# Performance work log

Measured on AMD Instinct MI355X. Metric: run time of the kernel, lower is better.

The kernel has to match this reference:

```python
import jax, jax.numpy as jnp
import numpy as np

EPS = 1e-8


def setup_inputs() -> dict:
    key = jax.random.key(0)
    ks = jax.random.split(key, 3)
    B, d_in, d_sae = 2048, 2048, 16384
    x = jax.random.normal(ks[0], (B, 2, d_in), dtype=jnp.float32)
    W_enc = jax.random.normal(ks[1], (d_in, d_sae), dtype=jnp.float32) / (d_in ** 0.5)
    W_dec = jax.random.normal(ks[2], (d_sae, d_in), dtype=jnp.float32) / (d_sae ** 0.5)
    b_enc = jnp.zeros((d_sae,), dtype=jnp.float32)
    b_dec = jnp.zeros((d_in,), dtype=jnp.float32)
    return {"x": x, "W_enc": W_enc, "W_dec": W_dec, "b_enc": b_enc,
            "b_dec": b_dec, "k": 64, "h": 8192}


def _encode(x, W_enc, b_enc, k):
    # x: (N, d_in) -> z: (N, d_sae), top-k sparsified with relu on kept values
    pre = x @ W_enc + b_enc
    v, i = jax.lax.top_k(pre, k)                       # (N, k)
    rows = jnp.arange(pre.shape[0])[:, None]
    return jnp.zeros_like(pre).at[rows, i].set(jax.nn.relu(v))


def _info_nce(z_a, z_b):
    z_a = z_a / jnp.maximum(jnp.linalg.norm(z_a, axis=-1, keepdims=True), EPS)
    z_b = z_b / jnp.maximum(jnp.linalg.norm(z_b, axis=-1, keepdims=True), EPS)
    sim = z_a @ z_b.T                                  # (B, B)
    diag = jnp.diagonal(sim)
    ce_row = jnp.mean(jax.nn.logsumexp(sim, axis=1) - diag)
    ce_col = jnp.mean(jax.nn.logsumexp(sim, axis=0) - diag)
    return 0.5 * (ce_row + ce_col)


def reference(x, W_enc, W_dec, b_enc, b_dec, k, h):
    alpha = 1.0
    B, _, d_in = x.shape
    # encode both tokens in one GEMM: (2B, d_in)
    x_flat = x.reshape(B * 2, d_in)
    z = _encode(x_flat, W_enc, b_enc, k)               # (2B, d_sae)
    x_hat_full = z @ W_dec + b_dec                     # (2B, d_in)
    x_hat_high = z[:, :h] @ W_dec[:h, :] + b_dec       # (2B, d_in)
    per_tok = d_in
    # mean over batch per token, summed over prev+cur (matches 4 separate means)
    se_full = jnp.sum((x_hat_full - x_flat) ** 2, axis=-1).reshape(B, 2)
    se_high = jnp.sum((x_hat_high - x_flat) ** 2, axis=-1).reshape(B, 2)
    l_matr = (jnp.mean(se_full, axis=0).sum() + jnp.mean(se_high, axis=0).sum()) / per_tok
    z2 = z.reshape(B, 2, -1)
    z_h_prev = z2[:, 0, :h]
    z_h_cur = z2[:, 1, :h]
    l_contr = _info_nce(z_h_cur, z_h_prev)
    total = l_matr + alpha * l_contr
    x_hat_cur = x_hat_full.reshape(B, 2, d_in)[:, 1]
    z_cur = z2[:, 1]
    return (total, x_hat_cur, z_cur)
```

## Files before the change

### kernel.cpp

```cpp
#include <hip/hip_runtime.h>
#include <hip/hip_bf16.h>
#include <math.h>

#define D_IN   2048
#define D_SAE  16384
#define NROWS  4096
#define KTOP   64
#define HDIM   8192
#define CHUNK  1024
#define EPSN   1e-8f
#define BANDW_F16 4e-3f
#define BANDW_F32 4e-4f
#define BANDCAP 512
#define NTILE   128
#define SEG     16
#define CAPT    (NTILE*SEG)
#define TH_CAND 2.0f

typedef unsigned short u16;
typedef unsigned char u8;
typedef _Float16 f16;
typedef __attribute__((ext_vector_type(8))) _Float16 f16x8;
typedef __attribute__((ext_vector_type(4))) _Float16 f16x4;
typedef __attribute__((ext_vector_type(8))) unsigned short u16x8;
typedef __attribute__((ext_vector_type(4))) float float4v;
typedef __attribute__((ext_vector_type(2))) float f32x2;

__device__ __forceinline__ unsigned f2u(float f) {
  unsigned b = __float_as_uint(f);
  return (b & 0x80000000u) ? ~b : (b | 0x80000000u);
}
__device__ __forceinline__ float u2f(unsigned u) {
  unsigned b = (u & 0x80000000u) ? (u & 0x7fffffffu) : ~u;
  return __uint_as_float(b);
}
__device__ __forceinline__ u16 f2bf_rne(float f) {
  unsigned b = __float_as_uint(f);
  unsigned r = (b + 0x7fffu + ((b >> 16) & 1u)) >> 16;
  return (u16)r;
}
__device__ __forceinline__ float bf2f(u16 u) {
  return __uint_as_float(((unsigned)u) << 16);
}
__device__ __forceinline__ void async_copy16(void* lds, const void* g) {
  __builtin_amdgcn_global_load_lds(
      (const __attribute__((address_space(1))) unsigned*)(g),
      (__attribute__((address_space(3))) unsigned*)(lds), 16, 0, 0);
}

__global__ __launch_bounds__(256)
void pre_kernel(const float* __restrict__ x, const float* __restrict__ W,
                f16* __restrict__ Axh, f16* __restrict__ Th,
                float* __restrict__ WT)
{
  __shared__ float S[64][65];
  const int bid = blockIdx.x;
  if (bid < 8192) {
    const int tx = threadIdx.x & 63, ty = threadIdx.x >> 6;
    const int n0 = (bid & 255) * 64, k0 = (bid >> 8) * 64;
#pragma unroll
    for (int i = 0; i < 16; ++i) {
      int kl = ty + i * 4;
      S[kl][tx] = W[(size_t)(k0 + kl) * D_SAE + n0 + tx];
    }
    __syncthreads();
#pragma unroll
    for (int i = 0; i < 16; ++i) {
      int nl = ty + i * 4;
      float v = S[tx][nl];
      Th[(size_t)(n0 + nl) * D_IN + k0 + tx] = (f16)v;
      WT[(size_t)(n0 + nl) * D_IN + k0 + tx] = v;
    }
  } else {
    int t = (bid - 8192) * 256 + threadIdx.x;
    const int n4 = (NROWS * D_IN) / 4;
    if (t < n4) {
      float4 v = ((const float4*)x)[t];
      f16x4 h;
      h.x = (f16)v.x; h.y = (f16)v.y; h.z = (f16)v.z; h.w = (f16)v.w;
      ((f16x4*)Axh)[t] = h;
    }
  }
}

__global__ __launch_bounds__(256)
void wdec_to_fp8_kernel(const float* __restrict__ W,
                        u8* __restrict__ W8, float* __restrict__ scl)
{
  __shared__ float red[256];
  const int c = blockIdx.x;
  const int tid = threadIdx.x;
  const int e0 = tid * 8;
  const float* wr = W + (size_t)c * 2048;
  float4 a = *(const float4*)(wr + e0);
  float4 b = *(const float4*)(wr + e0 + 4);
  float w[8] = {a.x,a.y,a.z,a.w,b.x,b.y,b.z,b.w};
  float mx = 0.f;
#pragma unroll
  for (int i = 0; i < 8; ++i) mx = fmaxf(mx, fabsf(w[i]));
  red[tid] = mx; __syncthreads();
  for (int s = 128; s > 0; s >>= 1) { if (tid < s) red[tid] = fmaxf(red[tid], red[tid+s]); __syncthreads(); }
  const float mxa = red[0];
  const float senc = mxa > 0.f ? 448.f / mxa : 0.f;
  float q[8];
#pragma unroll
  for (int i = 0; i < 8; ++i) q[i] = fminf(fmaxf(w[i] * senc, -448.f), 448.f);
  int p0 = __builtin_amdgcn_cvt_pk_fp8_f32(q[0], q[1], 0, false);
  p0 = __builtin_amdgcn_cvt_pk_fp8_f32(q[2], q[3], p0, true);
  int p1 = __builtin_amdgcn_cvt_pk_fp8_f32(q[4], q[5], 0, false);
  p1 = __builtin_amdgcn_cvt_pk_fp8_f32(q[6], q[7], p1, true);
  uint2 o; o.x = (unsigned)p0; o.y = (unsigned)p1;
  *(uint2*)(W8 + (size_t)c * 2048 + e0) = o;
  if (tid == 0) scl[c] = mxa > 0.f ? mxa / 448.f : 0.f;
}

__global__ __launch_bounds__(256, 4)
void gemm_f16_kernel(const f16* __restrict__ Axh,
                     const f16* __restrict__ BT,
                     const float* __restrict__ bias,
                     unsigned* __restrict__ ckey_g,
                     u16* __restrict__ cidx_g,
                     unsigned* __restrict__ ccnt)
{
  __shared__ u16 sA[2][128 * 32];
  __shared__ u16 sB[2][128 * 32];
  const int tid = threadIdx.x;
  const int wave = tid >> 6, lane = tid & 63;
  const int bid = blockIdx.x;
  const int chunk = bid >> 10;
  const int b10 = bid & 1023;
  const int xcd = b10 & 7, loc = b10 >> 3;
  const int n0 = (xcd * 16 + (loc >> 3)) * 128;
  const int m0 = (loc & 7) * 128;
  const int row_base = chunk * CHUNK;
  const f16* A = Axh + (size_t)chunk * CHUNK * D_IN;
  const int wm = (wave >> 1) * 64, wn = (wave & 1) * 64;
  const int fr = lane & 15, fkg = lane >> 4;

  float4v acc[4][4];
#pragma unroll
  for (int i = 0; i < 4; ++i)
#pragma unroll
    for (int j = 0; j < 4; ++j) acc[i][j] = (float4v){0.f, 0.f, 0.f, 0.f};

  int aoff[4], boff[4];
#pragma unroll
  for (int mi = 0; mi < 4; ++mi) {
    int r = wm + mi * 16 + fr;
    aoff[mi] = r * 32 + ((fkg ^ ((r >> 1) & 3)) * 8);
    int c = wn + mi * 16 + fr;
    boff[mi] = c * 32 + ((fkg ^ ((c >> 1) & 3)) * 8);
  }

  auto stage = [&](int b, int k0) {
#pragma unroll
    for (int i = 0; i < 4; ++i) {
      int n = (i * 4 + wave) * 64 + lane;
      if (n < 512) {
        int row = n >> 2, s = n & 3;
        int fg = s ^ ((row >> 1) & 3);
        async_copy16((char*)&sA[b][0] + (size_t)n * 16,
                     A + (size_t)(m0 + row) * D_IN + k0 + fg * 8);
      } else {
        int n2 = n - 512;
        int row = n2 >> 2, s = n2 & 3;
        int fg = s ^ ((row >> 1) & 3);
        async_copy16((char*)&sB[b][0] + (size_t)n2 * 16,
                     BT + (size_t)(n0 + row) * D_IN + k0 + fg * 8);
      }
    }
  };

  stage(0, 0);
  __syncthreads();
  for (int t = 0; t < 64; ++t) {
    const int cur = t & 1;
    if (t < 63) stage(cur ^ 1, (t + 1) * 32);
    f16x8 a[4], b[4];
#pragma unroll
    for (int mi = 0; mi < 4; ++mi)
      a[mi] = *(const f16x8*)&sA[cur][aoff[mi]];
#pragma unroll
    for (int ni = 0; ni < 4; ++ni)
      b[ni] = *(const f16x8*)&sB[cur][boff[ni]];
#pragma unroll
    for (int mi = 0; mi < 4; ++mi)
#pragma unroll
      for (int ni = 0; ni < 4; ++ni)
        acc[mi][ni] = __builtin_amdgcn_mfma_f32_16x16x32_f16(a[mi], b[ni], acc[mi][ni], 0, 0, 0);
    __syncthreads();
  }

  unsigned* lcnt = (unsigned*)&sA[0][0];
  if (tid < 128) lcnt[tid] = 0u;
  __syncthreads();
  const int tileIdx = n0 >> 7;
  const int orow = (lane >> 4) * 4;
#pragma unroll
  for (int mi = 0; mi < 4; ++mi) {
#pragma unroll
    for (int ni = 0; ni < 4; ++ni) {
      int col = n0 + wn + ni * 16 + fr;
      float bv = bias[col];
#pragma unroll
      for (int rr = 0; rr < 4; ++rr) {
        float val = acc[mi][ni][rr] + bv;
        if (val >= TH_CAND) {
          int lrow = wm + mi * 16 + orow + rr;
          unsigned j = atomicAdd(&lcnt[lrow], 1u);
          if (j < SEG) {
            size_t sb = ((size_t)(row_base + m0 + lrow) * NTILE + tileIdx) * SEG;
            ckey_g[sb + j] = f2u(val);
            cidx_g[sb + j] = (u16)col;
          }
        }
      }
    }
  }
  __syncthreads();
  if (tid < 128)
    ccnt[(size_t)(row_base + m0 + tid) * NTILE + tileIdx] = lcnt[tid];
}

__global__ __launch_bounds__(256)
void select_compact_kernel(const unsigned* __restrict__ ckey_g,
                           const u16* __restrict__ cidx_g,
                           const unsigned* __restrict__ ccnt,
                           const float* __restrict__ x,
                           const float* __restrict__ WT,
                           const float* __restrict__ benc,
                           float bandw,
                           int*   __restrict__ topk_idx,
                           float* __restrict__ topk_val,
                           float* __restrict__ nh_norm,
                           unsigned* __restrict__ flags)
{
  __shared__ unsigned ckey[CAPT];
  __shared__ u16      cidx[CAPT];
  __shared__ unsigned tof[128];
  __shared__ unsigned tc[128];
  __shared__ unsigned hist[256];
  __shared__ unsigned sscan[257];
  __shared__ unsigned wsum[4];
  __shared__ float    bv_l[64];
  __shared__ int      band_idx[BANDCAP];
  __shared__ float    band_val[BANDCAP];
  __shared__ double   band_ex[BANDCAP];
  __shared__ unsigned char picked[BANDCAP];
  __shared__ int      out_idx[64];
  __shared__ float    out_val[64];
  __shared__ float    sh_v64;
  __shared__ unsigned sh_mcnt, sh_bstar, sh_kth, sh_ocnt, sh_bcnt, sh_bad;

  const int tid = threadIdx.x;
  const int wv = tid >> 6, ln = tid & 63;
  const int r = blockIdx.x;

  if (tid == 0) { sh_ocnt = 0u; sh_bcnt = 0u; sh_bad = 0u; sh_mcnt = 0u; sh_bstar = 0xffffffffu; }
  hist[tid] = 0u;
  if (tid < 128) {
    unsigned c = ccnt[(size_t)r * NTILE + tid];
    tc[tid] = c;
    if (c > SEG) sh_bad = 1u;
  }
  __syncthreads();
  if (tid < 128) {
    unsigned v = tc[tid];
#pragma unroll
    for (int d = 1; d < 64; d <<= 1) {
      unsigned t = __shfl_up(v, d);
      if (ln >= d) v += t;
    }
    tof[tid] = v;
  }
  __syncthreads();
  if (tid >= 64 && tid < 128) tof[tid] += tof[63];
  __syncthreads();
  const unsigned cc_u = tof[127];
  const int cc = (int)(cc_u < CAPT ? cc_u : CAPT);

  {
    unsigned ck[8]; u16 ci[8]; unsigned pv[8];
#pragma unroll
    for (int b = 0; b < 8; ++b) {
      int idx = tid + 256 * b;
      int tile = idx >> 4, slot = idx & 15;
      unsigned c = tc[tile]; if (c > SEG) c = SEG;
      bool valid = (unsigned)slot < c;
      pv[b] = valid ? (tof[tile] - tc[tile] + slot) : 0xffffffffu;
      ck[b] = valid ? ckey_g[(size_t)r * CAPT + idx] : 0u;
      ci[b] = valid ? cidx_g[(size_t)r * CAPT + idx] : (u16)0;
    }
#pragma unroll
    for (int b = 0; b < 8; ++b) {
      if (pv[b] < (unsigned)CAPT) { ckey[pv[b]] = ck[b]; cidx[pv[b]] = ci[b]; }
    }
  }
  __syncthreads();

  bool bad = (sh_bad != 0u) || (cc_u < 64u) || (cc_u > (unsigned)CAPT);

  if (!bad) {
    for (int s = tid; s < cc; s += 256) {
      float v = u2f(ckey[s]);
      int b = (int)((v - TH_CAND) * 100.0f);
      b = b < 0 ? 0 : (b > 255 ? 255 : b);
      atomicAdd(&hist[b], 1u);
    }
  }
  __syncthreads();
  {
    int rt = 255 - tid;
    unsigned v = hist[rt];
#pragma unroll
    for (int d = 1; d < 64; d <<= 1) {
      unsigned t = __shfl_up(v, d);
      if (ln >= d) v += t;
    }
    if (ln == 63) wsum[wv] = v;
    __syncthreads();
    unsigned add = 0;
    for (int w = 0; w < wv; ++w) add += wsum[w];
    sscan[rt] = v + add;
    if (tid == 0) sscan[256] = 0u;
    __syncthreads();
    if (sscan[tid] >= 64u && sscan[tid + 1] < 64u) {
      sh_bstar = (unsigned)tid;
      sh_kth = 64u - sscan[tid + 1];
    }
  }
  __syncthreads();

  if (bad || sh_bstar == 0xffffffffu) { if (tid == 0) flags[r] = 1u; return; }
  const int bstar = (int)sh_bstar;
  const unsigned kth = sh_kth;

  for (int s = tid; s < cc; s += 256) {
    float v = u2f(ckey[s]);
    int b = (int)((v - TH_CAND) * 100.0f);
    b = b < 0 ? 0 : (b > 255 ? 255 : b);
    if (b == bstar) {
      unsigned p = atomicAdd(&sh_mcnt, 1u);
      if (p < 64u) bv_l[p] = v;
    }
  }
  __syncthreads();
  if (sh_mcnt > 64u) { if (tid == 0) flags[r] = 1u; return; }
  const int m = (int)sh_mcnt;
  if (wv == 0 && ln < m) {
    float mine = bv_l[ln];
    int rank = 0;
    for (int j = 0; j < m; ++j) {
      float o = bv_l[j];
      if (o > mine || (o == mine && j < ln)) ++rank;
    }
    if (rank == (int)kth - 1) sh_v64 = mine;
  }
  __syncthreads();
  const float v64 = sh_v64;

  const float hi = v64 + 2.f * bandw, lo = v64 - 2.f * bandw;
  for (int s = tid; s < cc; s += 256) {
    float v = u2f(ckey[s]);
    int i = (int)cidx[s];
    if (v > hi) {
      unsigned p = atomicAdd(&sh_ocnt, 1u);
      out_idx[p] = i; out_val[p] = v;
    } else if (v >= lo) {
      unsigned p = atomicAdd(&sh_bcnt, 1u);
      if (p < BANDCAP) { band_idx[p] = i; band_val[p] = v; }
    }
  }
  __syncthreads();
  if (sh_bcnt > BANDCAP) { if (tid == 0) flags[r] = 1u; return; }
  const unsigned nci = sh_ocnt;
  const unsigned bcnt = sh_bcnt;
  const unsigned remaining = 64u - nci;

  if (bcnt == remaining) {
    for (unsigned s = tid; s < bcnt; s += 256) {
      out_idx[nci + s] = band_idx[s];
      out_val[nci + s] = band_val[s];
    }
    __syncthreads();
  } else {
    const float* xr = x + (size_t)r * 2048;
    for (unsigned bi = wv; bi < bcnt; bi += 4) {
      int c = band_idx[bi];
      const float* wr = WT + (size_t)c * 2048;
      double s = 0.0;
      for (int j0 = 0; j0 < 2048; j0 += 512) {
        float xa[8], wa[8];
#pragma unroll
        for (int u = 0; u < 8; ++u) {
          int j = j0 + ln + 64 * u;
          xa[u] = xr[j];
          wa[u] = wr[j];
        }
#pragma unroll
        for (int u = 0; u < 8; ++u)
          s += (double)xa[u] * (double)wa[u];
      }
#pragma unroll
      for (int off2 = 32; off2 > 0; off2 >>= 1)
        s += __shfl_down(s, off2);
      if (ln == 0) band_ex[bi] = s + (double)benc[c];
    }
    __syncthreads();
    if (tid == 0) {
      for (unsigned i2 = 0; i2 < bcnt; ++i2) picked[i2] = 0;
      for (unsigned s = 0; s < remaining; ++s) {
        int best = -1;
        for (unsigned b2 = 0; b2 < bcnt; ++b2) {
          if (picked[b2]) continue;
          if (best < 0 || band_ex[b2] > band_ex[best] ||
              (band_ex[b2] == band_ex[best] && band_idx[b2] < band_idx[best]))
            best = (int)b2;
        }
        picked[best] = 1;
        out_idx[nci + s] = band_idx[best];
        out_val[nci + s] = (float)band_ex[best];
      }
    }
    __syncthreads();
  }

  if (tid < 64) {
    float v = out_val[tid];
    v = v > 0.f ? v : 0.f;
    out_val[tid] = v;
    topk_idx[(size_t)r * 64 + tid] = out_idx[tid];
    topk_val[(size_t)r * 64 + tid] = v;
  }
  __syncthreads();
  if (tid == 0) {
    float n2 = 0.f;
    for (int s = 0; s < 64; ++s)
      if (out_idx[s] < HDIM) n2 += out_val[s] * out_val[s];
    nh_norm[r] = sqrtf(n2);
    flags[r] = 0u;
  }
}

__global__ __launch_bounds__(256)
void repair_kernel(const unsigned* __restrict__ flags,
                   const float* __restrict__ x,
                   const float* __restrict__ WT,
                   const float* __restrict__ benc,
                   int* __restrict__ topk_idx,
                   float* __restrict__ topk_val,
                   float* __restrict__ nh_norm)
{
  const int r = blockIdx.x;
  if (flags[r] == 0u) return;
  __shared__ float prerow[16384];
  __shared__ float xs[2048];
  __shared__ float rv[256];
  __shared__ int   ri[256];
  __shared__ int   oi[64];
  __shared__ float ov[64];
  const int tid = threadIdx.x;
  for (int i = tid; i < 2048; i += 256) xs[i] = x[(size_t)r * 2048 + i];
  __syncthreads();
  for (int c = tid; c < 16384; c += 256) {
    const float* wr = WT + (size_t)c * 2048;
    float s = 0.f;
    for (int j = 0; j < 2048; ++j) s = fmaf(xs[j], wr[j], s);
    prerow[c] = s + benc[c];
  }
  __syncthreads();
  for (int k2 = 0; k2 < 64; ++k2) {
    float bv = -INFINITY; int bi = 16384;
    for (int c = tid; c < 16384; c += 256) {
      float v = prerow[c];
      if (v > bv || (v == bv && c < bi)) { bv = v; bi = c; }
    }
    rv[tid] = bv; ri[tid] = bi;
    __syncthreads();
    for (int s2 = 128; s2 > 0; s2 >>= 1) {
      if (tid < s2) {
        if (rv[tid+s2] > rv[tid] || (rv[tid+s2] == rv[tid] && ri[tid+s2] < ri[tid])) {
          rv[tid] = rv[tid+s2]; ri[tid] = ri[tid+s2];
        }
      }
      __syncthreads();
    }
    if (tid == 0) { oi[k2] = ri[0]; ov[k2] = rv[0]; prerow[ri[0]] = -INFINITY; }
    __syncthreads();
  }
  if (tid < 64) {
    float v = ov[tid]; v = v > 0.f ? v : 0.f;
    topk_idx[(size_t)r * 64 + tid] = oi[tid];
    topk_val[(size_t)r * 64 + tid] = v;
  }
  __syncthreads();
  if (tid == 0) {
    float n2 = 0.f;
    for (int s = 0; s < 64; ++s)
      if (oi[s] < HDIM) { float v = ov[s] > 0.f ? ov[s] : 0.f; n2 += v * v; }
    nh_norm[r] = sqrtf(n2);
  }
}

__global__ __launch_bounds__(256)
void scatter_kernel(const int* __restrict__ topk_idx,
                    const float* __restrict__ topk_val,
                    const float* __restrict__ nh_norm,
                    float* __restrict__ zcur_out,
                    u16* __restrict__ ZpTb)
{
  int t = blockIdx.x * blockDim.x + threadIdx.x;
  if (t >= NROWS * 64) return;
  int r = t >> 6;
  int c = topk_idx[t];
  float v = topk_val[t];
  int b = r >> 1;
  if (r & 1) {
    zcur_out[(size_t)b * 16384 + c] = v;
  } else if (c < HDIM) {
    float nrm = nh_norm[r]; nrm = nrm > EPSN ? nrm : EPSN;
    ZpTb[(size_t)c * 2048 + b] = f2bf_rne(v / nrm);
  }
}

__global__ __launch_bounds__(256)
void token_kernel(const int* __restrict__ topk_idx,
                  const float* __restrict__ topk_val,
                  const u8* __restrict__ W8,
                  const float* __restrict__ scl,
                  const float* __restrict__ bdec,
                  const float* __restrict__ x,
                  const float* __restrict__ nh_norm,
                  const u16* __restrict__ ZpTb,
                  float* __restrict__ se_full,
                  float* __restrict__ se_high,
                  float* __restrict__ xhat_out,
                  float* __restrict__ simb,
                  float* __restrict__ lse_row,
                  float* __restrict__ diag)
{
  __shared__ int sidx[64];
  __shared__ float sval[64];
  __shared__ float red[256];
  __shared__ int cidx2[64];
  __shared__ float cval2[64];
  __shared__ int scnt;
  const int tid = threadIdx.x;
  const int r = blockIdx.x;
  const int e0 = tid * 8;
  if (tid == 0) scnt = 0;
  if (tid < 64) {
    int c = topk_idx[(size_t)r*64+tid];
    sidx[tid] = c;
    sval[tid] = topk_val[(size_t)r*64+tid] * scl[c];
  }
  __syncthreads();
  float accf[8], acch[8];
  {
    float4 b0 = *(const float4*)(bdec + e0);
    float4 b1 = *(const float4*)(bdec + e0 + 4);
    accf[0]=b0.x; accf[1]=b0.y; accf[2]=b0.z; accf[3]=b0.w;
    accf[4]=b1.x; accf[5]=b1.y; accf[6]=b1.z; accf[7]=b1.w;
#pragma unroll
    for (int i = 0; i < 8; ++i) acch[i] = accf[i];
  }
  for (int s0 = 0; s0 < 64; s0 += 8) {
    uint2 w[8]; float vf[8], vh[8];
#pragma unroll
    for (int j = 0; j < 8; ++j) {
      int c = sidx[s0 + j];
      float v = sval[s0 + j];
      vf[j] = v;
      vh[j] = (c < HDIM) ? v : 0.f;
      w[j] = *(const uint2*)(W8 + (size_t)c * 2048 + e0);
    }
#pragma unroll
    for (int j = 0; j < 8; ++j) {
      f32x2 f0 = __builtin_amdgcn_cvt_pk_f32_fp8((int)w[j].x, false);
      f32x2 f1 = __builtin_amdgcn_cvt_pk_f32_fp8((int)w[j].x, true);
      f32x2 f2 = __builtin_amdgcn_cvt_pk_f32_fp8((int)w[j].y, false);
      f32x2 f3 = __builtin_amdgcn_cvt_pk_f32_fp8((int)w[j].y, true);
      float wvv[8] = {f0[0],f0[1],f1[0],f1[1],f2[0],f2[1],f3[0],f3[1]};
#pragma unroll
      for (int i = 0; i < 8; ++i) {
        accf[i] = fmaf(vf[j], wvv[i], accf[i]);
        acch[i] = fmaf(vh[j], wvv[i], acch[i]);
      }
    }
  }
  const float* xr = x + (size_t)r * 2048;
  float4 x0 = *(const float4*)(xr + e0);
  float4 x1 = *(const float4*)(xr + e0 + 4);
  float xv[8] = {x0.x,x0.y,x0.z,x0.w,x1.x,x1.y,x1.z,x1.w};
  float sf = 0.f, shs = 0.f;
#pragma unroll
  for (int i = 0; i < 8; ++i) {
    float df = accf[i] - xv[i]; sf += df*df;
    float dh = acch[i] - xv[i]; shs += dh*dh;
  }
  red[tid] = sf; __syncthreads();
  for (int s2=128; s2>0; s2>>=1){ if (tid<s2) red[tid]+=red[tid+s2]; __syncthreads(); }
  if (tid==0) se_full[r] = red[0];
  __syncthreads();
  red[tid] = shs; __syncthreads();
  for (int s2=128; s2>0; s2>>=1){ if (tid<s2) red[tid]+=red[tid+s2]; __syncthreads(); }
  if (tid==0) se_high[r] = red[0];
  if (!(r & 1)) return;

  {
    float* orow = xhat_out + (size_t)(r >> 1) * 2048;
    float4 o0 = {accf[0],accf[1],accf[2],accf[3]};
    float4 o1 = {accf[4],accf[5],accf[6],accf[7]};
    *(float4*)(orow + e0) = o0;
    *(float4*)(orow + e0 + 4) = o1;
  }
  const int i = r >> 1;
  __syncthreads();
  if (tid < 64) {
    int c = sidx[tid];
    float v = topk_val[(size_t)r*64+tid];
    if (c < HDIM) {
      float nrm = nh_norm[r]; nrm = nrm > EPSN ? nrm : EPSN;
      int p = atomicAdd(&scnt, 1);
      cidx2[p] = c; cval2[p] = v / nrm;
    }
  }
  __syncthreads();
  float acc[8];
#pragma unroll
  for (int ii = 0; ii < 8; ++ii) acc[ii] = 0.f;
  const int m = scnt;
  int s = 0;
  for (; s + 8 <= m; s += 8) {
    u16x8 z[8]; float vv[8];
#pragma unroll
    for (int j = 0; j < 8; ++j) {
      vv[j] = cval2[s + j];
      z[j] = *(const u16x8*)(ZpTb + (size_t)cidx2[s + j] * 2048 + e0);
    }
#pragma unroll
    for (int j = 0; j < 8; ++j)
#pragma unroll
      for (int ii = 0; ii < 8; ++ii)
        acc[ii] = fmaf(vv[j], bf2f(z[j][ii]), acc[ii]);
  }
  for (; s < m; ++s) {
    int c = cidx2[s]; float v = cval2[s];
    u16x8 z8 = *(const u16x8*)(ZpTb + (size_t)c * 2048 + e0);
#pragma unroll
    for (int ii = 0; ii < 8; ++ii)
      acc[ii] = fmaf(v, bf2f(z8[ii]), acc[ii]);
  }
  {
    float* srow = simb + (size_t)i * 2048;
    float4 o0 = {acc[0],acc[1],acc[2],acc[3]};
    float4 o1 = {acc[4],acc[5],acc[6],acc[7]};
    *(float4*)(srow + e0) = o0;
    *(float4*)(srow + e0 + 4) = o1;
  }
  float mx = -INFINITY;
#pragma unroll
  for (int ii = 0; ii < 8; ++ii) mx = fmaxf(mx, acc[ii]);
  if ((i >> 3) == tid) diag[i] = acc[i & 7];
  red[tid] = mx; __syncthreads();
  for (int s2=128; s2>0; s2>>=1){ if (tid<s2) red[tid]=fmaxf(red[tid],red[tid+s2]); __syncthreads(); }
  mx = red[0]; __syncthreads();
  float se = 0.f;
#pragma unroll
  for (int ii = 0; ii < 8; ++ii) se += expf(acc[ii] - mx);
  red[tid] = se; __syncthreads();
  for (int s2=128; s2>0; s2>>=1){ if (tid<s2) red[tid]+=red[tid+s2]; __syncthreads(); }
  if (tid == 0) lse_row[i] = mx + logf(red[0]);
}

__global__ __launch_bounds__(256)
void gemm_pre_kernel(const float* __restrict__ A,
                     const float* __restrict__ B,
                     const float* __restrict__ bias,
                     float* __restrict__ C)
{
  __shared__ float As[16][129];
  __shared__ float Bs[16][129];
  const int tid = threadIdx.x;
  const int tx = tid & 15, ty = tid >> 4;
  const int m0 = blockIdx.y * 128;
  const int n0 = blockIdx.x * 128;
  float acc[8][8];
#pragma unroll
  for (int i = 0; i < 8; ++i)
#pragma unroll
    for (int j = 0; j < 8; ++j) acc[i][j] = 0.f;
  const int lk = tid & 15, lm = tid >> 4;
  for (int k0 = 0; k0 < 2048; k0 += 16) {
#pragma unroll
    for (int i = 0; i < 8; ++i) {
      int m = lm + 16 * i;
      As[lk][m] = A[(size_t)(m0 + m) * 2048 + k0 + lk];
    }
#pragma unroll
    for (int i = 0; i < 8; ++i) {
      int idx = tid + 256 * i;
      int kk = idx >> 7, nn = idx & 127;
      Bs[kk][nn] = B[(size_t)(k0 + kk) * 16384 + n0 + nn];
    }
    __syncthreads();
#pragma unroll
    for (int kk = 0; kk < 16; ++kk) {
      float a[8], b[8];
#pragma unroll
      for (int i = 0; i < 8; ++i) a[i] = As[kk][ty + 16 * i];
#pragma unroll
      for (int j = 0; j < 8; ++j) b[j] = Bs[kk][tx + 16 * j];
#pragma unroll
      for (int i = 0; i < 8; ++i)
#pragma unroll
        for (int j = 0; j < 8; ++j) acc[i][j] = fmaf(a[i], b[j], acc[i][j]);
    }
    __syncthreads();
  }
#pragma unroll
  for (int i = 0; i < 8; ++i) {
    int m = m0 + ty + 16 * i;
#pragma unroll
    for (int j = 0; j < 8; ++j) {
      int n = n0 + tx + 16 * j;
      C[(size_t)m * 16384 + n] = acc[i][j] + bias[n];
    }
  }
}

__global__ __launch_bounds__(256)
void select_fb_kernel(const float* __restrict__ pre,
                      const float* __restrict__ x,
                      const float* __restrict__ Wenc,
                      const float* __restrict__ benc,
                      int row_base, float bandw,
                      int*   __restrict__ topk_idx,
                      float* __restrict__ topk_val,
                      float* __restrict__ nh_norm)
{
  __shared__ unsigned hist[256];
  __shared__ int      band_idx[BANDCAP];
  __shared__ double   band_ex[BANDCAP];
  __shared__ double   red_d[256];
  __shared__ int      out_idx[64];
  __shared__ float    out_val[64];
  __shared__ unsigned char picked[BANDCAP];
  __shared__ unsigned sh_prefix, sh_need, sh_ocnt, sh_bcnt;

  const int tid = threadIdx.x;
  const int lrow = blockIdx.x;
  const int row = row_base + lrow;
  const float* prow = pre + (size_t)lrow * 16384;

  if (tid == 0) { sh_prefix = 0u; sh_need = 64u; }
  __syncthreads();
  for (int level = 24; level >= 0; level -= 8) {
    hist[tid] = 0u;
    __syncthreads();
    unsigned prefix = sh_prefix;
    for (int i = tid; i < 16384; i += 256) {
      unsigned u = f2u(prow[i]);
      bool match = (level == 24) || ((u >> ((level + 8) & 31)) == prefix);
      if (match) atomicAdd(&hist[(u >> level) & 255u], 1u);
    }
    __syncthreads();
    if (tid == 0) {
      unsigned need = sh_need, acc = 0; int q = 0;
      for (int b2 = 255; b2 >= 0; --b2) {
        if (acc + hist[b2] >= need) { q = b2; break; }
        acc += hist[b2];
      }
      sh_prefix = (prefix << 8) | (unsigned)q;
      sh_need = need - acc;
    }
    __syncthreads();
  }
  const float v64 = u2f(sh_prefix);

  if (tid == 0) { sh_ocnt = 0u; sh_bcnt = 0u; }
  __syncthreads();
  const float hi = v64 + 2.f * bandw, lo = v64 - 2.f * bandw;
  for (int i = tid; i < 16384; i += 256) {
    float v = prow[i];
    if (v > hi) {
      unsigned p = atomicAdd(&sh_ocnt, 1u);
      out_idx[p] = i; out_val[p] = v;
    } else if (v >= lo) {
      unsigned p = atomicAdd(&sh_bcnt, 1u);
      if (p < BANDCAP) { band_idx[p] = i; }
    }
  }
  __syncthreads();
  const unsigned nci = sh_ocnt;
  const unsigned bcnt = sh_bcnt < BANDCAP ? sh_bcnt : BANDCAP;
  const unsigned remaining = 64u - nci;

  if (bcnt == remaining) {
    for (unsigned s = tid; s < bcnt; s += 256) {
      int c = band_idx[s];
      out_idx[nci + s] = c;
      out_val[nci + s] = prow[c];
    }
    __syncthreads();
  } else {
    const float* xr = x + (size_t)row * 2048;
    for (unsigned bi = 0; bi < bcnt; ++bi) {
      int c = band_idx[bi];
      double part = 0.0;
#pragma unroll
      for (int j2 = 0; j2 < 8; ++j2) {
        int kk = tid + 256 * j2;
        part += (double)xr[kk] * (double)Wenc[(size_t)kk * 16384 + c];
      }
      red_d[tid] = part;
      __syncthreads();
      for (int sft = 128; sft > 0; sft >>= 1) {
        if (tid < sft) red_d[tid] += red_d[tid + sft];
        __syncthreads();
      }
      if (tid == 0) band_ex[bi] = red_d[0] + (double)benc[c];
      __syncthreads();
    }
    if (tid == 0) {
      for (unsigned i2 = 0; i2 < bcnt; ++i2) picked[i2] = 0;
      for (unsigned s = 0; s < remaining; ++s) {
        int best = -1;
        for (unsigned b2 = 0; b2 < bcnt; ++b2) {
          if (picked[b2]) continue;
          if (best < 0 || band_ex[b2] > band_ex[best] ||
              (band_ex[b2] == band_ex[best] && band_idx[b2] < band_idx[best]))
            best = (int)b2;
        }
        picked[best] = 1;
        out_idx[nci + s] = band_idx[best];
        out_val[nci + s] = (float)band_ex[best];
      }
    }
    __syncthreads();
  }

  if (tid < 64) {
    float v = out_val[tid];
    v = v > 0.f ? v : 0.f;
    out_val[tid] = v;
    topk_idx[(size_t)row * 64 + tid] = out_idx[tid];
    topk_val[(size_t)row * 64 + tid] = v;
  }
  __syncthreads();
  if (tid == 0) {
    float n2 = 0.f;
    for (int s = 0; s < 64; ++s)
      if (out_idx[s] < HDIM) n2 += out_val[s] * out_val[s];
    nh_norm[row] = sqrtf(n2);
  }
}

__global__ __launch_bounds__(256)
void scatter_f32_kernel(const int* __restrict__ topk_idx,
                        const float* __restrict__ topk_val,
                        const float* __restrict__ nh_norm,
                        float* __restrict__ zcur_out,
                        float* __restrict__ ZpT)
{
  int t = blockIdx.x * blockDim.x + threadIdx.x;
  if (t >= NROWS * 64) return;
  int r = t >> 6;
  int c = topk_idx[t];
  float v = topk_val[t];
  int b = r >> 1;
  if (r & 1) {
    zcur_out[(size_t)b * 16384 + c] = v;
  } else if (c < HDIM) {
    float nrm = nh_norm[r]; nrm = nrm > EPSN ? nrm : EPSN;
    ZpT[(size_t)c * 2048 + b] = v / nrm;
  }
}

__global__ __launch_bounds__(256)
void decode_f32_kernel(const int* __restrict__ topk_idx,
                       const float* __restrict__ topk_val,
                       const float* __restrict__ Wdec,
                       const float* __restrict__ bdec,
                       const float* __restrict__ x,
                       float* __restrict__ se_full,
                       float* __restrict__ se_high,
                       float* __restrict__ xhat_out)
{
  __shared__ int sidx[64];
  __shared__ float sval[64];
  __shared__ float red[256];
  const int tid = threadIdx.x;
  const int r = blockIdx.x;
  if (tid < 64) { sidx[tid] = topk_idx[(size_t)r*64+tid]; sval[tid] = topk_val[(size_t)r*64+tid]; }
  __syncthreads();
  float accf[8], acch[8];
#pragma unroll
  for (int i = 0; i < 8; ++i) { float b = bdec[tid + 256*i]; accf[i] = b; acch[i] = b; }
  for (int s = 0; s < 64; ++s) {
    int c = sidx[s]; float v = sval[s];
    const float* wr = Wdec + (size_t)c * 2048;
    bool high = (c < HDIM);
#pragma unroll
    for (int i = 0; i < 8; ++i) {
      float w = wr[tid + 256*i];
      accf[i] = fmaf(v, w, accf[i]);
      if (high) acch[i] = fmaf(v, w, acch[i]);
    }
  }
  const float* xr = x + (size_t)r * 2048;
  float sf = 0.f, shs = 0.f;
#pragma unroll
  for (int i = 0; i < 8; ++i) {
    float xv = xr[tid + 256*i];
    float df = accf[i] - xv; sf += df*df;
    float dh = acch[i] - xv; shs += dh*dh;
  }
  red[tid] = sf; __syncthreads();
  for (int s2=128; s2>0; s2>>=1){ if (tid<s2) red[tid]+=red[tid+s2]; __syncthreads(); }
  if (tid==0) se_full[r] = red[0];
  __syncthreads();
  red[tid] = shs; __syncthreads();
  for (int s2=128; s2>0; s2>>=1){ if (tid<s2) red[tid]+=red[tid+s2]; __syncthreads(); }
  if (tid==0) se_high[r] = red[0];
  if (r & 1) {
    float* orow = xhat_out + (size_t)(r >> 1) * 2048;
#pragma unroll
    for (int i = 0; i < 8; ++i) orow[tid + 256*i] = accf[i];
  }
}

__global__ __launch_bounds__(256)
void sim_f32_kernel(const int* __restrict__ topk_idx,
                    const float* __restrict__ topk_val,
                    const float* __restrict__ nh_norm,
                    const float* __restrict__ ZpT,
                    float* __restrict__ sim)
{
  __shared__ int cidx2[64];
  __shared__ float cval2[64];
  __shared__ int scnt;
  const int tid = threadIdx.x;
  const int i = blockIdx.x;
  const int r = 2 * i + 1;
  if (tid == 0) scnt = 0;
  __syncthreads();
  if (tid < 64) {
    int c = topk_idx[(size_t)r*64+tid];
    float v = topk_val[(size_t)r*64+tid];
    if (c < HDIM) {
      float nrm = nh_norm[r]; nrm = nrm > EPSN ? nrm : EPSN;
      int p = atomicAdd(&scnt, 1);
      cidx2[p] = c; cval2[p] = v / nrm;
    }
  }
  __syncthreads();
  float acc[8];
#pragma unroll
  for (int ii = 0; ii < 8; ++ii) acc[ii] = 0.f;
  int m = scnt;
  for (int s = 0; s < m; ++s) {
    int c = cidx2[s]; float v = cval2[s];
    const float* zr = ZpT + (size_t)c * 2048;
#pragma unroll
    for (int ii = 0; ii < 8; ++ii)
      acc[ii] = fmaf(v, zr[tid + 256*ii], acc[ii]);
  }
  float* srow = sim + (size_t)i * 2048;
#pragma unroll
  for (int ii = 0; ii < 8; ++ii) srow[tid + 256*ii] = acc[ii];
}

__global__ __launch_bounds__(256)
void lse_row_kernel(const float* __restrict__ sim,
                    float* __restrict__ lse_row, float* __restrict__ diag)
{
  __shared__ float red[256];
  const int tid = threadIdx.x; const int i = blockIdx.x;
  const int e0 = tid * 8;
  const float* srow = sim + (size_t)i * 2048;
  float4 v0 = *(const float4*)(srow + e0);
  float4 v1 = *(const float4*)(srow + e0 + 4);
  float vals[8] = {v0.x,v0.y,v0.z,v0.w,v1.x,v1.y,v1.z,v1.w};
  float mx = -INFINITY;
#pragma unroll
  for (int ii=0; ii<8; ++ii) mx = fmaxf(mx, vals[ii]);
  if ((i >> 3) == tid) diag[i] = vals[i & 7];
  red[tid]=mx; __syncthreads();
  for (int s=128;s>0;s>>=1){ if (tid<s) red[tid]=fmaxf(red[tid],red[tid+s]); __syncthreads(); }
  mx = red[0]; __syncthreads();
  float se=0.f;
#pragma unroll
  for (int ii=0;ii<8;++ii) se += expf(vals[ii]-mx);
  red[tid]=se; __syncthreads();
  for (int s=128;s>0;s>>=1){ if (tid<s) red[tid]+=red[tid+s]; __syncthreads(); }
  if (tid==0) lse_row[i] = mx + logf(red[0]);
}

__global__ __launch_bounds__(256)
void lse_col_kernel(const float* __restrict__ sim, float* __restrict__ lse_col)
{
  __shared__ float ml[32][9], sl[32][9];
  const int tid = threadIdx.x;
  const int c = tid & 7, rr = tid >> 3;
  const int col = blockIdx.x * 8 + c;
  float m = -INFINITY, s = 0.f;
  for (int r = rr; r < 2048; r += 32) {
    float v = sim[(size_t)r * 2048 + col];
    float mn = fmaxf(m, v);
    s = s * expf(m - mn) + expf(v - mn);
    m = mn;
  }
  ml[rr][c] = m; sl[rr][c] = s;
  __syncthreads();
  if (rr == 0) {
    float M = ml[0][c];
#pragma unroll
    for (int i = 1; i < 32; ++i) M = fmaxf(M, ml[i][c]);
    float S = 0.f;
#pragma unroll
    for (int i = 0; i < 32; ++i) S += sl[i][c] * expf(ml[i][c] - M);
    lse_col[col] = M + logf(S);
  }
}

__global__ __launch_bounds__(256)
void final_kernel(const float* __restrict__ se_full, const float* __restrict__ se_high,
                  const float* __restrict__ lse_row, const float* __restrict__ lse_col,
                  const float* __restrict__ diag, float* __restrict__ out0)
{
  __shared__ float red[256];
  const int tid = threadIdx.x;
  float s1 = 0.f;
  for (int i = tid; i < 4096; i += 256) s1 += se_full[i] + se_high[i];
  red[tid]=s1; __syncthreads();
  for (int s=128;s>0;s>>=1){ if (tid<s) red[tid]+=red[tid+s]; __syncthreads(); }
  float matr = red[0]; __syncthreads();
  float s2 = 0.f;
  for (int i = tid; i < 2048; i += 256) s2 += (lse_row[i]-diag[i]) + (lse_col[i]-diag[i]);
  red[tid]=s2; __syncthreads();
  for (int s=128;s>0;s>>=1){ if (tid<s) red[tid]+=red[tid+s]; __syncthreads(); }
  if (tid == 0) {
    float l_matr  = matr / (2048.f * 2048.f);
    float l_contr = 0.5f * (red[0] / 2048.f);
    out0[0] = l_matr + l_contr;
  }
}

extern "C" void kernel_launch(void* const* d_in, const int* in_sizes, int n_in,
                              void* d_out, int out_size, void* d_ws, size_t ws_size,
                              hipStream_t stream)
{
  const float* x    = (const float*)d_in[0];
  const float* Wenc = (const float*)d_in[1];
  const float* Wdec = (const float*)d_in[2];
  const float* benc = (const float*)d_in[3];
  const float* bdec = (const float*)d_in[4];
  float* out = (float*)d_out;
  float* xhat_out = out + 1;
  float* zcur_out = out + 1 + (size_t)2048 * 2048;
  (void)in_sizes; (void)n_in; (void)out_size;

  char* ws = (char*)d_ws;
  size_t off = 0;
  auto alloc = [&](size_t bytes) {
    char* p = ws + off; off += (bytes + 255) & ~(size_t)255; return p;
  };
  int*      tki     = (int*)     alloc((size_t)NROWS * 64 * 4);
  float*    tkv     = (float*)   alloc((size_t)NROWS * 64 * 4);
  float*    nh_norm = (float*)   alloc((size_t)NROWS * 4);
  float*    se_f    = (float*)   alloc((size_t)NROWS * 4);
  float*    se_h    = (float*)   alloc((size_t)NROWS * 4);
  float*    lse_r   = (float*)   alloc((size_t)2048 * 4);
  float*    lse_c   = (float*)   alloc((size_t)2048 * 4);
  float*    diag    = (float*)   alloc((size_t)2048 * 4);
  f16*      Axh     = (f16*)     alloc((size_t)NROWS * D_IN * 2);
  unsigned* ckey_g  = (unsigned*)alloc((size_t)NROWS * CAPT * 4);
  u16*      cidx_g  = (u16*)     alloc((size_t)NROWS * CAPT * 2);
  unsigned* ccnt    = (unsigned*)alloc((size_t)NROWS * NTILE * 4);
  unsigned* flags   = (unsigned*)alloc((size_t)NROWS * 4);
  char*     R1      = alloc((size_t)D_SAE * D_IN * 2);
  char*     R2      = alloc((size_t)D_SAE * D_IN * 4);
  size_t need = off;

  f16*   Th    = (f16*)R1;
  u8*    W8    = (u8*)R1;
  float* scl   = (float*)(R1 + (size_t)D_SAE * D_IN);
  float* WT    = (float*)R2;
  u16*   ZpTb  = (u16*)R2;
  float* simb  = (float*)(R2 + (size_t)8192 * 2048 * 2);

  hipMemsetAsync(zcur_out, 0, (size_t)2048 * 16384 * 4, stream);

  if (ws_size >= need) {
    pre_kernel<<<16384, 256, 0, stream>>>(x, Wenc, Axh, Th, WT);
    gemm_f16_kernel<<<4096, 256, 0, stream>>>(Axh, Th, benc, ckey_g, cidx_g, ccnt);
    select_compact_kernel<<<NROWS, 256, 0, stream>>>(ckey_g, cidx_g, ccnt, x, WT, benc,
        BANDW_F16, tki, tkv, nh_norm, flags);
    repair_kernel<<<NROWS, 256, 0, stream>>>(flags, x, WT, benc, tki, tkv, nh_norm);
    wdec_to_fp8_kernel<<<D_SAE, 256, 0, stream>>>(Wdec, W8, scl);
    hipMemsetAsync(ZpTb, 0, (size_t)8192 * 2048 * 2, stream);
    scatter_kernel<<<(NROWS * 64) / 256, 256, 0, stream>>>(tki, tkv, nh_norm, zcur_out, ZpTb);
    token_kernel<<<NROWS, 256, 0, stream>>>(tki, tkv, W8, scl, bdec, x, nh_norm, ZpTb,
        se_f, se_h, xhat_out, simb, lse_r, diag);
    lse_col_kernel<<<256, 256, 0, stream>>>(simb, lse_c);
    final_kernel<<<1, 256, 0, stream>>>(se_f, se_h, lse_r, lse_c, diag, out);
  } else {
    off = 0;
    float* pre2  = (float*)alloc((size_t)CHUNK * 16384 * 4);
    int*   tki2  = (int*)  alloc((size_t)NROWS * 64 * 4);
    float* tkv2  = (float*)alloc((size_t)NROWS * 64 * 4);
    float* nh2   = (float*)alloc((size_t)NROWS * 4);
    float* sef2  = (float*)alloc((size_t)NROWS * 4);
    float* seh2  = (float*)alloc((size_t)NROWS * 4);
    float* lr2   = (float*)alloc((size_t)2048 * 4);
    float* lc2   = (float*)alloc((size_t)2048 * 4);
    float* dg2   = (float*)alloc((size_t)2048 * 4);
    float* ZpT2  = (float*)alloc((size_t)8192 * 2048 * 4);
    float* sim2  = (float*)alloc((size_t)2048 * 2048 * 4);
    for (int ch = 0; ch < 4; ++ch) {
      dim3 g(128, 8);
      gemm_pre_kernel<<<g, 256, 0, stream>>>(x + (size_t)ch * CHUNK * 2048, Wenc, benc, pre2);
      select_fb_kernel<<<CHUNK, 256, 0, stream>>>(pre2, x, Wenc, benc,
          ch * CHUNK, BANDW_F32, tki2, tkv2, nh2);
    }
    hipMemsetAsync(ZpT2, 0, (size_t)8192 * 2048 * 4, stream);
    scatter_f32_kernel<<<(NROWS * 64) / 256, 256, 0, stream>>>(tki2, tkv2, nh2, zcur_out, ZpT2);
    decode_f32_kernel<<<NROWS, 256, 0, stream>>>(tki2, tkv2, Wdec, bdec, x, sef2, seh2, xhat_out);
    sim_f32_kernel<<<2048, 256, 0, stream>>>(tki2, tkv2, nh2, ZpT2, sim2);
    lse_row_kernel<<<2048, 256, 0, stream>>>(sim2, lr2, dg2);
    lse_col_kernel<<<256, 256, 0, stream>>>(sim2, lc2);
    final_kernel<<<1, 256, 0, stream>>>(sef2, seh2, lr2, lc2, dg2, out);
  }
}
```

Baseline: 719.5 us.

## Use 256x256 tiles with 512 threads and interleaved prefetch in encoder GEMM

Restructures the f16 encoder GEMM from 128x128 tiles with 256 threads to 256x256 tiles with 8 waves, each wave computing 128x64. The K loop now stages 64-wide slices split into two 32-wide halves, issues async copies between MFMA groups, and waits with explicit vmcnt and s_setprio. This raises arithmetic intensity per shared-memory load and cuts global traffic, at the cost of more registers (128 accumulator floats per lane) and 128KB of LDS, which limits occupancy. The candidate-emission epilogue is adapted so each block covers two 128-column tiles.

```diff
diff --git a/kernel.cpp b/kernel.cpp
--- a/kernel.cpp
+++ b/kernel.cpp
@@ -114,7 +114,7 @@
   if (tid == 0) scl[c] = mxa > 0.f ? mxa / 448.f : 0.f;
 }
 
-__global__ __launch_bounds__(256, 4)
+__global__ __launch_bounds__(512, 2)
 void gemm_f16_kernel(const f16* __restrict__ Axh,
                      const f16* __restrict__ BT,
                      const float* __restrict__ bias,
@@ -122,94 +122,145 @@
                      u16* __restrict__ cidx_g,
                      unsigned* __restrict__ ccnt)
 {
-  __shared__ u16 sA[2][128 * 32];
-  __shared__ u16 sB[2][128 * 32];
-  const int tid = threadIdx.x;
+  __shared__ u16 As[2][2][256 * 32];
+  __shared__ u16 Bs[2][2][256 * 32];
+  const int tid  = threadIdx.x;
   const int wave = tid >> 6, lane = tid & 63;
-  const int bid = blockIdx.x;
-  const int chunk = bid >> 10;
-  const int b10 = bid & 1023;
-  const int xcd = b10 & 7, loc = b10 >> 3;
-  const int n0 = (xcd * 16 + (loc >> 3)) * 128;
-  const int m0 = (loc & 7) * 128;
-  const int row_base = chunk * CHUNK;
-  const f16* A = Axh + (size_t)chunk * CHUNK * D_IN;
-  const int wm = (wave >> 1) * 64, wn = (wave & 1) * 64;
-  const int fr = lane & 15, fkg = lane >> 4;
-
-  float4v acc[4][4];
-#pragma unroll
-  for (int i = 0; i < 4; ++i)
+  const int bid  = blockIdx.x;
+  const int xcd  = bid & 7, loc = bid >> 3;
+  const int n0   = (xcd * 8 + (loc >> 4)) * 256;
+  const int m0   = (loc & 15) * 256;
+  const int wr   = wave >> 2;
+  const int wc   = wave & 3;
+  const int fr   = lane & 15;
+  const int fsl  = lane >> 4;
+
+  float4v acc[8][4];
+#pragma unroll
+  for (int i = 0; i < 8; ++i)
 #pragma unroll
     for (int j = 0; j < 4; ++j) acc[i][j] = (float4v){0.f, 0.f, 0.f, 0.f};
 
-  int aoff[4], boff[4];
-#pragma unroll
-  for (int mi = 0; mi < 4; ++mi) {
-    int r = wm + mi * 16 + fr;
-    aoff[mi] = r * 32 + ((fkg ^ ((r >> 1) & 3)) * 8);
-    int c = wn + mi * 16 + fr;
-    boff[mi] = c * 32 + ((fkg ^ ((c >> 1) & 3)) * 8);
-  }
-
-  auto stage = [&](int b, int k0) {
-#pragma unroll
-    for (int i = 0; i < 4; ++i) {
-      int n = (i * 4 + wave) * 64 + lane;
-      if (n < 512) {
-        int row = n >> 2, s = n & 3;
-        int fg = s ^ ((row >> 1) & 3);
-        async_copy16((char*)&sA[b][0] + (size_t)n * 16,
-                     A + (size_t)(m0 + row) * D_IN + k0 + fg * 8);
-      } else {
-        int n2 = n - 512;
-        int row = n2 >> 2, s = n2 & 3;
-        int fg = s ^ ((row >> 1) & 3);
-        async_copy16((char*)&sB[b][0] + (size_t)n2 * 16,
-                     BT + (size_t)(n0 + row) * D_IN + k0 + fg * 8);
+  int aoff[8], boff[4];
+#pragma unroll
+  for (int mi = 0; mi < 8; ++mi) {
+    int row = wr * 128 + mi * 16 + fr;
+    aoff[mi] = row * 32 + ((fsl ^ ((row >> 1) & 3)) * 8);
+  }
+#pragma unroll
+  for (int n = 0; n < 4; ++n) {
+    int col = wc * 64 + n * 16 + fr;
+    boff[n] = col * 32 + ((fsl ^ ((col >> 1) & 3)) * 8);
+  }
+
+  auto stA = [&](int bf, int tt, int ks, int half) {
+    int idx = half * 512 + tid;
+    int row = idx >> 2, sl = idx & 3;
+    int gc = tt * 64 + ks * 32 + ((sl ^ ((row >> 1) & 3)) * 8);
+    async_copy16((char*)&As[bf][ks][0] + (size_t)idx * 16,
+                 Axh + (size_t)(m0 + row) * D_IN + gc);
+  };
+  auto stB = [&](int bf, int tt, int ks, int half) {
+    int idx = half * 512 + tid;
+    int row = idx >> 2, sl = idx & 3;
+    int gc = tt * 64 + ks * 32 + ((sl ^ ((row >> 1) & 3)) * 8);
+    async_copy16((char*)&Bs[bf][ks][0] + (size_t)idx * 16,
+                 BT + (size_t)(n0 + row) * D_IN + gc);
+  };
+
+  stA(0, 0, 0, 0); stA(0, 0, 0, 1); stB(0, 0, 0, 0); stB(0, 0, 0, 1);
+  stA(0, 0, 1, 0); stA(0, 0, 1, 1); stB(0, 0, 1, 0); stB(0, 0, 1, 1);
+  asm volatile("s_waitcnt vmcnt(4)" ::: "memory");
+  __builtin_amdgcn_s_barrier();
+
+  for (int t = 0; t < 32; ++t) {
+    const int buf = t & 1, nbf = buf ^ 1;
+    const bool st = (t < 31);
+#pragma unroll
+    for (int ks = 0; ks < 2; ++ks) {
+      const u16* Ak = &As[buf][ks][0];
+      const u16* Bk = &Bs[buf][ks][0];
+      f16x8 b0 = *(const f16x8*)&Bk[boff[0]];
+      f16x8 b1 = *(const f16x8*)&Bk[boff[1]];
+      f16x8 b2 = *(const f16x8*)&Bk[boff[2]];
+      f16x8 b3 = *(const f16x8*)&Bk[boff[3]];
+      f16x8 a0 = *(const f16x8*)&Ak[aoff[0]];
+      f16x8 a1 = *(const f16x8*)&Ak[aoff[1]];
+      f16x8 a2 = *(const f16x8*)&Ak[aoff[2]];
+      f16x8 a3 = *(const f16x8*)&Ak[aoff[3]];
+      if (st) { stA(nbf, t + 1, ks, 0); stA(nbf, t + 1, ks, 1); }
+      __builtin_amdgcn_s_setprio(1);
+      acc[0][0] = __builtin_amdgcn_mfma_f32_16x16x32_f16(a0, b0, acc[0][0], 0, 0, 0);
+      acc[0][1] = __builtin_amdgcn_mfma_f32_16x16x32_f16(a0, b1, acc[0][1], 0, 0, 0);
+      acc[0][2] = __builtin_amdgcn_mfma_f32_16x16x32_f16(a0, b2, acc[0][2], 0, 0, 0);
+      acc[0][3] = __builtin_amdgcn_mfma_f32_16x16x32_f16(a0, b3, acc[0][3], 0, 0, 0);
+      acc[1][0] = __builtin_amdgcn_mfma_f32_16x16x32_f16(a1, b0, acc[1][0], 0, 0, 0);
+      acc[1][1] = __builtin_amdgcn_mfma_f32_16x16x32_f16(a1, b1, acc[1][1], 0, 0, 0);
+      acc[1][2] = __builtin_amdgcn_mfma_f32_16x16x32_f16(a1, b2, acc[1][2], 0, 0, 0);
+      acc[1][3] = __builtin_amdgcn_mfma_f32_16x16x32_f16(a1, b3, acc[1][3], 0, 0, 0);
+      acc[2][0] = __builtin_amdgcn_mfma_f32_16x16x32_f16(a2, b0, acc[2][0], 0, 0, 0);
+      acc[2][1] = __builtin_amdgcn_mfma_f32_16x16x32_f16(a2, b1, acc[2][1], 0, 0, 0);
+      acc[2][2] = __builtin_amdgcn_mfma_f32_16x16x32_f16(a2, b2, acc[2][2], 0, 0, 0);
+      acc[2][3] = __builtin_amdgcn_mfma_f32_16x16x32_f16(a2, b3, acc[2][3], 0, 0, 0);
+      acc[3][0] = __builtin_amdgcn_mfma_f32_16x16x32_f16(a3, b0, acc[3][0], 0, 0, 0);
+      acc[3][1] = __builtin_amdgcn_mfma_f32_16x16x32_f16(a3, b1, acc[3][1], 0, 0, 0);
+      acc[3][2] = __builtin_amdgcn_mfma_f32_16x16x32_f16(a3, b2, acc[3][2], 0, 0, 0);
+      acc[3][3] = __builtin_amdgcn_mfma_f32_16x16x32_f16(a3, b3, acc[3][3], 0, 0, 0);
+      __builtin_amdgcn_s_setprio(0);
+      a0 = *(const f16x8*)&Ak[aoff[4]];
+      a1 = *(const f16x8*)&Ak[aoff[5]];
+      a2 = *(const f16x8*)&Ak[aoff[6]];
+      a3 = *(const f16x8*)&Ak[aoff[7]];
+      if (st) { stB(nbf, t + 1, ks, 0); stB(nbf, t + 1, ks, 1); }
+      __builtin_amdgcn_s_setprio(1);
+      acc[4][0] = __builtin_amdgcn_mfma_f32_16x16x32_f16(a0, b0, acc[4][0], 0, 0, 0);
+      acc[4][1] = __builtin_amdgcn_mfma_f32_16x16x32_f16(a0, b1, acc[4][1], 0, 0, 0);
+      acc[4][2] = __builtin_amdgcn_mfma_f32_16x16x32_f16(a0, b2, acc[4][2], 0, 0, 0);
+      acc[4][3] = __builtin_amdgcn_mfma_f32_16x16x32_f16(a0, b3, acc[4][3], 0, 0, 0);
+      acc[5][0] = __builtin_amdgcn_mfma_f32_16x16x32_f16(a1, b0, acc[5][0], 0, 0, 0);
+      acc[5][1] = __builtin_amdgcn_mfma_f32_16x16x32_f16(a1, b1, acc[5][1], 0, 0, 0);
+      acc[5][2] = __builtin_amdgcn_mfma_f32_16x16x32_f16(a1, b2, acc[5][2], 0, 0, 0);
+      acc[5][3] = __builtin_amdgcn_mfma_f32_16x16x32_f16(a1, b3, acc[5][3], 0, 0, 0);
+      acc[6][0] = __builtin_amdgcn_mfma_f32_16x16x32_f16(a2, b0, acc[6][0], 0, 0, 0);
+      acc[6][1] = __builtin_amdgcn_mfma_f32_16x16x32_f16(a2, b1, acc[6][1], 0, 0, 0);
+      acc[6][2] = __builtin_amdgcn_mfma_f32_16x16x32_f16(a2, b2, acc[6][2], 0, 0, 0);
+      acc[6][3] = __builtin_amdgcn_mfma_f32_16x16x32_f16(a2, b3, acc[6][3], 0, 0, 0);
+      acc[7][0] = __builtin_amdgcn_mfma_f32_16x16x32_f16(a3, b0, acc[7][0], 0, 0, 0);
+      acc[7][1] = __builtin_amdgcn_mfma_f32_16x16x32_f16(a3, b1, acc[7][1], 0, 0, 0);
+      acc[7][2] = __builtin_amdgcn_mfma_f32_16x16x32_f16(a3, b2, acc[7][2], 0, 0, 0);
+      acc[7][3] = __builtin_amdgcn_mfma_f32_16x16x32_f16(a3, b3, acc[7][3], 0, 0, 0);
+      __builtin_amdgcn_s_setprio(0);
+      if (st) {
+        asm volatile("s_waitcnt vmcnt(4)" ::: "memory");
+        __builtin_amdgcn_s_barrier();
+      } else if (ks == 0) {
+        asm volatile("s_waitcnt vmcnt(0)" ::: "memory");
+        __builtin_amdgcn_s_barrier();
       }
     }
-  };
-
-  stage(0, 0);
-  __syncthreads();
-  for (int t = 0; t < 64; ++t) {
-    const int cur = t & 1;
-    if (t < 63) stage(cur ^ 1, (t + 1) * 32);
-    f16x8 a[4], b[4];
-#pragma unroll
-    for (int mi = 0; mi < 4; ++mi)
-      a[mi] = *(const f16x8*)&sA[cur][aoff[mi]];
-#pragma unroll
-    for (int ni = 0; ni < 4; ++ni)
-      b[ni] = *(const f16x8*)&sB[cur][boff[ni]];
-#pragma unroll
-    for (int mi = 0; mi < 4; ++mi)
-#pragma unroll
-      for (int ni = 0; ni < 4; ++ni)
-        acc[mi][ni] = __builtin_amdgcn_mfma_f32_16x16x32_f16(a[mi], b[ni], acc[mi][ni], 0, 0, 0);
-    __syncthreads();
-  }
-
-  unsigned* lcnt = (unsigned*)&sA[0][0];
-  if (tid < 128) lcnt[tid] = 0u;
-  __syncthreads();
-  const int tileIdx = n0 >> 7;
+  }
+  __syncthreads();
+
+  unsigned* lcnt = (unsigned*)&As[0][0][0];
+  lcnt[tid] = 0u;
+  __syncthreads();
+  const int tl = wc >> 1;
+  const int tileG = (n0 >> 7) + tl;
   const int orow = (lane >> 4) * 4;
 #pragma unroll
-  for (int mi = 0; mi < 4; ++mi) {
-#pragma unroll
-    for (int ni = 0; ni < 4; ++ni) {
-      int col = n0 + wn + ni * 16 + fr;
+  for (int mi = 0; mi < 8; ++mi) {
+#pragma unroll
+    for (int nj = 0; nj < 4; ++nj) {
+      int col = n0 + wc * 64 + nj * 16 + fr;
       float bv = bias[col];
 #pragma unroll
       for (int rr = 0; rr < 4; ++rr) {
-        float val = acc[mi][ni][rr] + bv;
+        float val = acc[mi][nj][rr] + bv;
         if (val >= TH_CAND) {
-          int lrow = wm + mi * 16 + orow + rr;
-          unsigned j = atomicAdd(&lcnt[lrow], 1u);
+          int lrow = wr * 128 + mi * 16 + orow + rr;
+          unsigned j = atomicAdd(&lcnt[tl * 256 + lrow], 1u);
           if (j < SEG) {
-            size_t sb = ((size_t)(row_base + m0 + lrow) * NTILE + tileIdx) * SEG;
+            size_t sb = ((size_t)(m0 + lrow) * NTILE + tileG) * SEG;
             ckey_g[sb + j] = f2u(val);
             cidx_g[sb + j] = (u16)col;
           }
@@ -218,8 +269,7 @@
     }
   }
   __syncthreads();
-  if (tid < 128)
-    ccnt[(size_t)(row_base + m0 + tid) * NTILE + tileIdx] = lcnt[tid];
+  ccnt[(size_t)(m0 + (tid & 255)) * NTILE + (n0 >> 7) + (tid >> 8)] = lcnt[tid];
 }
 
 __global__ __launch_bounds__(256)
@@ -1094,7 +1144,7 @@
 
   if (ws_size >= need) {
     pre_kernel<<<16384, 256, 0, stream>>>(x, Wenc, Axh, Th, WT);
-    gemm_f16_kernel<<<4096, 256, 0, stream>>>(Axh, Th, benc, ckey_g, cidx_g, ccnt);
+    gemm_f16_kernel<<<1024, 512, 0, stream>>>(Axh, Th, benc, ckey_g, cidx_g, ccnt);
     select_compact_kernel<<<NROWS, 256, 0, stream>>>(ckey_g, cidx_g, ccnt, x, WT, benc,
         BANDW_F16, tki, tkv, nh_norm, flags);
     repair_kernel<<<NROWS, 256, 0, stream>>>(flags, x, WT, benc, tki, tkv, nh_norm);
```

Measured after the change: 696.7 us. -3.2%, faster.
